# Optimization experiments

Hardware: AMD Instinct MI355X
Metric: run time of the kernel (lower is better)

Reference implementation:

```python
import jax, jax.numpy as jnp
import numpy as np
import math

IN_STACKS, IN_DIM, OUT_DIM = 4, 256, 2048
N_TOK = 16384


def _beta(a, b):
    return math.exp(math.lgamma(a) + math.lgamma(b) - math.lgamma(a + b))

BETA_NI = _beta(IN_DIM / 2.0, 0.5)
BETA_N = _beta(IN_DIM * IN_STACKS / 2.0, 0.5)


def sabs(x, eps=1e-15):
    return jnp.maximum(jnp.abs(x), eps)


def _project(x, k, eps=0.004):  # fp32 eps per source
    maxnorm = (1.0 - eps) / jnp.sqrt(sabs(k))
    maxnorm = jnp.where(k < 0, maxnorm, jnp.asarray(1e15, x.dtype))
    norm = jnp.maximum(jnp.linalg.norm(x, axis=-1, keepdims=True), 1e-15)
    return jnp.where(norm > maxnorm, x / norm * maxnorm, x)


def arsinh(x):
    return jnp.log(jnp.maximum(x + jnp.sqrt(1.0 + x * x), 1e-15))


def expmap0(u, c):
    sqrt_c = jnp.sqrt(c)
    un = jnp.maximum(jnp.linalg.norm(u, axis=-1, keepdims=True), 1e-15)
    gamma = jnp.tanh(sqrt_c * un) * u / (sqrt_c * un)
    return _project(gamma, -c)


def logmap0(y, c):
    sqrt_c = jnp.sqrt(c)
    yn = jnp.maximum(jnp.linalg.norm(y, axis=-1, keepdims=True), 1e-15)
    arg = jnp.minimum(sqrt_c * yn, 1.0 - 1e-7)
    return y / (sqrt_c * yn) * jnp.arctanh(arg)


def unidirectional_poincare_mlr(x, z_norm, z_unit, r, c):
    rc = jnp.sqrt(c)
    drcr = 2.0 * rc * r  # [out_dim]
    rcx = rc * x  # [N, D]
    cx2 = jnp.sum(rcx * rcx, axis=-1, keepdims=True)  # [N, 1]
    num = 2.0 * jnp.matmul(rcx, z_unit) * jnp.cosh(drcr) - (1.0 + cx2) * jnp.sinh(drcr)
    return 2.0 * z_norm / rc * arsinh(num / jnp.maximum(1.0 - cx2, 1e-15))


def poincare_linear(x, weight_g, z_unit, bias, c):
    rc = jnp.sqrt(c)
    y = unidirectional_poincare_mlr(x, weight_g, z_unit, bias, c)
    y = jnp.sinh(rc * y) / rc
    denom = 1.0 + jnp.sqrt(1.0 + c * jnp.sum(y * y, axis=-1, keepdims=True))
    return _project(y / denom, -c)


def setup_inputs() -> dict:
    key = jax.random.key(0)
    k1, k2 = jax.random.split(key)
    x = jax.random.normal(k1, (N_TOK, IN_STACKS, IN_DIM), dtype=jnp.float32)
    std = 1.0 / (2.0 * IN_DIM * IN_STACKS * OUT_DIM) ** 0.5
    weight_v = jax.random.normal(k2, (IN_STACKS * IN_DIM, OUT_DIM), dtype=jnp.float32) * std
    weight_g = jnp.linalg.norm(weight_v, axis=0)  # [OUT_DIM]
    bias = jnp.zeros((OUT_DIM,), dtype=jnp.float32)
    c = jnp.asarray(1.0, dtype=jnp.float32)
    return {"x": x, "weight_g": weight_g, "weight_v": weight_v, "bias": bias, "c": c}


def reference(x, weight_g, weight_v, bias, c):
    # x: [N, in_stacks, in_dim]
    xb = expmap0(x, c)
    xb = logmap0(xb, c).reshape(x.shape[0], IN_STACKS * IN_DIM)
    xb = expmap0(xb * (BETA_N / BETA_NI), c)
    z_unit = weight_v / jnp.maximum(jnp.linalg.norm(weight_v, axis=0), 1e-15)
    return poincare_linear(xb, weight_g, z_unit, bias, c)
```

## Files before the change

kernel.cpp:

```cpp
#include <hip/hip_runtime.h>
#include <hip/hip_bf16.h>
#include <hip/hip_fp16.h>
#include <cmath>

#define NTOK 16384
#define KDIM 1024
#define NDIM 2048
#define NSTK 4
#define SDIM 256

typedef __attribute__((ext_vector_type(8))) _Float16 f16x8;
typedef __attribute__((ext_vector_type(4))) float f32x4;

static __device__ __forceinline__ unsigned short f2h(float f) {
  union { _Float16 h; unsigned short u; } v;
  v.h = (_Float16)f;
  return v.u;
}

#define ASCL 16.0f
#define BSCL 32.0f
#define ABSCL 512.0f

__global__ void prep_cols(const float* __restrict__ wg, const float* __restrict__ bias,
                          const float* __restrict__ cptr, float* __restrict__ colp) {
  int j = blockIdx.x * 256 + threadIdx.x;
  if (j >= NDIM) return;
  float c = cptr[0];
  float rc = sqrtf(c);
  float w = wg[j];
  float invn = 1.0f / fmaxf(w, 1e-15f);
  float drcr = 2.0f * rc * bias[j];
  float ed = expf(drcr);
  float edi = 1.0f / ed;
  float coshd = 0.5f * (ed + edi);
  float sinhd = 0.5f * (ed - edi);
  colp[4 * j + 0] = 2.0f * invn * coshd / ABSCL;
  colp[4 * j + 1] = sinhd;
  colp[4 * j + 2] = 2.0f * w;
  colp[4 * j + 3] = 0.0f;
}

__global__ void transpose_w(const float* __restrict__ wv, unsigned short* __restrict__ Bt) {
  __shared__ float tile[32][33];
  int n0 = blockIdx.x * 32;
  int k0 = blockIdx.y * 32;
  int tx = threadIdx.x;
  int ty = threadIdx.y;
  for (int i = 0; i < 32; i += 8)
    tile[ty + i][tx] = wv[(long)(k0 + ty + i) * NDIM + n0 + tx];
  __syncthreads();
  for (int i = 0; i < 32; i += 8)
    Bt[(long)(n0 + ty + i) * KDIM + k0 + tx] = f2h(tile[tx][ty + i] * BSCL);
}

__global__ __launch_bounds__(256) void prep_x(const float* __restrict__ x, const float* __restrict__ cptr,
                                              unsigned short* __restrict__ A, float* __restrict__ cx2out,
                                              float Rbeta) {
  int w = threadIdx.x >> 6, lane = threadIdx.x & 63;
  int tok = blockIdx.x * 4 + w;
  const float4* x4 = (const float4*)x;
  float4 v[NSTK];
  float ss[NSTK];
  for (int s = 0; s < NSTK; s++) {
    float4 t = x4[(long)tok * 256 + s * 64 + lane];
    v[s] = t;
    float d = t.x * t.x + t.y * t.y + t.z * t.z + t.w * t.w;
    for (int m = 1; m < 64; m <<= 1) d += __shfl_xor(d, m);
    ss[s] = d;
  }
  float c = cptr[0];
  float rc = sqrtf(c);
  float h[NSTK], un[NSTK], hs2 = 0.0f;
  for (int s = 0; s < NSTK; s++) {
    un[s] = fmaxf(sqrtf(ss[s]), 1e-15f);
    float t1 = fminf(tanhf(rc * un[s]), 0.996f);
    float z = fminf(t1, 1.0f - 1e-7f);
    float hh = 0.5f * logf((1.0f + z) / (1.0f - z));
    h[s] = hh;
    hs2 += hh * hh;
  }
  float sqh = sqrtf(hs2);
  float uwrc = Rbeta * sqh;
  float t2 = fminf(tanhf(uwrc), 0.996f);
  if (lane == 0) cx2out[tok] = t2 * t2;
  float denomw = fmaxf(uwrc, rc * 1e-15f);
  for (int s = 0; s < NSTK; s++) {
    float scl = ASCL * Rbeta * h[s] * t2 / (un[s] * denomw);
    float4 t = v[s];
    ushort4 pk = make_ushort4(f2h(t.x * scl), f2h(t.y * scl), f2h(t.z * scl), f2h(t.w * scl));
    *(ushort4*)&A[(long)tok * KDIM + s * SDIM + lane * 4] = pk;
  }
}

#define BK 64
#define NKT (KDIM / BK)

#define GLDS16(g, l)                                                              \
  __builtin_amdgcn_global_load_lds((const __attribute__((address_space(1))) void*)(g), \
                                   (__attribute__((address_space(3))) void*)(l), 16, 0, 0)

#define PH_BARRIER __builtin_amdgcn_s_barrier()
#define PRIO1 __builtin_amdgcn_s_setprio(1)
#define PRIO0 __builtin_amdgcn_s_setprio(0)
#define LGKM0                                                  \
  do {                                                         \
    asm volatile("s_waitcnt lgkmcnt(0)" ::: "memory");         \
    __builtin_amdgcn_sched_barrier(0);                         \
  } while (0)
#define VMCNT4 asm volatile("s_waitcnt vmcnt(4)" ::: "memory")
#define VMCNT0 asm volatile("s_waitcnt vmcnt(0)" ::: "memory")

#define ISSUE_A(T, H)                                                        \
  do {                                                                       \
    const unsigned short* _s = Asrc + (long)(H) * (128 * KDIM) + (T) * BK;   \
    unsigned char* _d = lds + (((T) & 1) * 32768 + (H) * 16384) + tid * 16;  \
    GLDS16(_s, _d);                                                          \
    GLDS16(_s + 64 * KDIM, _d + 8192);                                       \
  } while (0)
#define ISSUE_B(T, H)                                                        \
  do {                                                                       \
    const unsigned short* _s = Bsrc + (long)(H) * (128 * KDIM) + (T) * BK;   \
    unsigned char* _d = lds + 65536 + (((T) & 1) * 32768 + (H) * 16384) + tid * 16; \
    GLDS16(_s, _d);                                                          \
    GLDS16(_s + 64 * KDIM, _d + 8192);                                       \
  } while (0)

#define READ_A4(BUFOFF, FMB, KS)                                             \
  _Pragma("unroll") for (int fm = 0; fm < 4; ++fm)                           \
    aF[fm][KS] = *(const f16x8*)(lds + (BUFOFF) + aBase + ((FMB) + fm) * 2048 + chunk[KS]);
#define READ_B4(BUFOFF, KS)                                                  \
  _Pragma("unroll") for (int fn = 0; fn < 4; ++fn)                           \
    bF[fn][KS] = *(const f16x8*)(lds + 65536 + (BUFOFF) + bBase + fn * 2048 + chunk[KS]);

#define MFMA_PH(FM0, KS)                                                     \
  _Pragma("unroll") for (int fi = 0; fi < 4; ++fi)                           \
    _Pragma("unroll") for (int fj = 0; fj < 4; ++fj)                         \
      acc[(FM0) + fi][fj] = __builtin_amdgcn_mfma_f32_16x16x32_f16(          \
          aF[fi][KS], bF[fj][KS], acc[(FM0) + fi][fj], 0, 0, 0);

#define TILE(BUFOFF, T, GA, GB, VMODE)                                       \
  do {                                                                       \
    READ_A4(BUFOFF, 0, 0); READ_B4(BUFOFF, 0);                               \
    if (GA) ISSUE_A((T) + 1, 0);                                             \
    PH_BARRIER; LGKM0;                                                       \
    PRIO1; MFMA_PH(0, 0); PRIO0;                                             \
    PH_BARRIER;                                                              \
    READ_A4(BUFOFF, 0, 1); READ_B4(BUFOFF, 1);                               \
    if (GA) ISSUE_A((T) + 1, 1);                                             \
    PH_BARRIER; LGKM0;                                                       \
    PRIO1; MFMA_PH(0, 1); PRIO0;                                             \
    PH_BARRIER;                                                              \
    READ_A4(BUFOFF, 4, 0);                                                   \
    if (GB) ISSUE_B((T) + 2, 0);                                             \
    PH_BARRIER; LGKM0;                                                       \
    PRIO1; MFMA_PH(4, 0); PRIO0;                                             \
    PH_BARRIER;                                                              \
    READ_A4(BUFOFF, 4, 1);                                                   \
    if (GB) ISSUE_B((T) + 2, 1);                                             \
    if ((VMODE) == 0) { VMCNT4; } else if ((VMODE) == 1) { VMCNT0; }         \
    PH_BARRIER; LGKM0;                                                       \
    PRIO1; MFMA_PH(4, 1); PRIO0;                                             \
    PH_BARRIER;                                                              \
  } while (0)

template <int F16S>
__global__ __launch_bounds__(512, 2) void gemm_ep(const unsigned short* __restrict__ A,
                                                  const unsigned short* __restrict__ Bt,
                                                  const float* __restrict__ cx2,
                                                  const float* __restrict__ colp,
                                                  const float* __restrict__ cptr,
                                                  float* __restrict__ outY,
                                                  unsigned short* __restrict__ y16,
                                                  float* __restrict__ partials) {
  __shared__ __attribute__((aligned(16))) unsigned char lds[131072];
  int tid = threadIdx.x;
  int lane = tid & 63, w = tid >> 6;
  int wm = w >> 2, wn = w & 3;
  int g = lane >> 4, r = lane & 15;
  int bid = blockIdx.x;
  int tile_n = bid & 7, tile_m = bid >> 3;
  int m0 = tile_m * 256, n0 = tile_n * 256;

  int srow = tid >> 3;
  int csrc = ((tid & 7) ^ (srow & 7)) << 3;
  const unsigned short* Asrc = A + (long)(m0 + srow) * KDIM + csrc;
  const unsigned short* Bsrc = Bt + (long)(n0 + srow) * KDIM + csrc;

  int aBase = wm * 16384 + r * 128;
  int bBase = (wn >> 1) * 16384 + (wn & 1) * 8192 + r * 128;
  int chunk[2];
  chunk[0] = ((0 * 4 + g) ^ (r & 7)) * 16;
  chunk[1] = ((1 * 4 + g) ^ (r & 7)) * 16;

  f32x4 acc[8][4];
#pragma unroll
  for (int i = 0; i < 8; i++)
#pragma unroll
    for (int j = 0; j < 4; j++) acc[i][j] = (f32x4){0.f, 0.f, 0.f, 0.f};
  f16x8 aF[4][2], bF[4][2];

  ISSUE_A(0, 0); ISSUE_A(0, 1); ISSUE_B(0, 0); ISSUE_B(0, 1);
  ISSUE_B(1, 0); ISSUE_B(1, 1);
  VMCNT4;
  PH_BARRIER;

#pragma unroll 1
  for (int it = 0; it < 7; ++it) {
    TILE(0, 2 * it, 1, 1, 0);
    TILE(32768, 2 * it + 1, 1, 1, 0);
  }
  TILE(0, 14, 1, 0, 1);
  TILE(32768, 15, 0, 0, 2);

  float c = cptr[0];
  float rc = sqrtf(c);
  float inv_rc = 1.0f / rc;
  const float4* cp4 = (const float4*)colp;
  int tn4 = tile_n * 4 + wn;
#pragma unroll
  for (int fm = 0; fm < 8; ++fm) {
#pragma unroll
    for (int q = 0; q < 4; ++q) {
      int row = m0 + wm * 128 + fm * 16 + g * 4 + q;
      float cx = cx2[row];
      float onec = 1.0f + cx;
      float rdn = 1.0f / fmaxf(1.0f - cx, 1e-15f);
      float rs = 0.0f;
#pragma unroll
      for (int fn = 0; fn < 4; ++fn) {
        int col = n0 + wn * 64 + fn * 16 + r;
        float4 cp = cp4[col];
        float dot = acc[fm][fn][q];
        float num = fmaf(dot, cp.x, -onec * cp.y);
        float u = num * rdn;
        float au = fabsf(u);
        float as = __logf(au + sqrtf(fmaf(au, au, 1.0f)));
        as = copysignf(as, u);
        float s2 = cp.z * as;
        float ex = __expf(s2);
        float exi = __builtin_amdgcn_rcpf(ex);
        float y = 0.5f * (ex - exi) * inv_rc;
        if (F16S)
          y16[(long)row * NDIM + col] = f2h(y);
        else
          outY[(long)row * NDIM + col] = y;
        rs = fmaf(y, y, rs);
      }
      rs += __shfl_xor(rs, 1);
      rs += __shfl_xor(rs, 2);
      rs += __shfl_xor(rs, 4);
      rs += __shfl_xor(rs, 8);
      if (r == 0) partials[(long)row * 32 + tn4] = rs;
    }
  }
}

__global__ __launch_bounds__(256) void finalize16(const unsigned short* __restrict__ y16,
                                                  const float* __restrict__ partials,
                                                  const float* __restrict__ cptr,
                                                  float* __restrict__ out) {
  int w = threadIdx.x >> 6, lane = threadIdx.x & 63;
  int row = blockIdx.x * 4 + w;
  float p = (lane < 32) ? partials[(long)row * 32 + lane] : 0.0f;
  for (int m = 1; m < 64; m <<= 1) p += __shfl_xor(p, m);
  float c = cptr[0];
  float S = p;
  float denom = 1.0f + sqrtf(fmaf(c, S, 1.0f));
  float nv = fmaxf(sqrtf(S) / denom, 1e-15f);
  float maxn = (c > 0.0f) ? 0.996f / sqrtf(fmaxf(c, 1e-15f)) : 1e15f;
  float scl = (nv > maxn) ? (maxn / (nv * denom)) : (1.0f / denom);
  const f16x8* yr = (const f16x8*)(y16 + (long)row * NDIM);
  float4* o4 = (float4*)(out + (long)row * NDIM);
#pragma unroll
  for (int it = 0; it < 4; ++it) {
    f16x8 v = yr[it * 64 + lane];
    float4 a, b;
    a.x = (float)v[0] * scl; a.y = (float)v[1] * scl;
    a.z = (float)v[2] * scl; a.w = (float)v[3] * scl;
    b.x = (float)v[4] * scl; b.y = (float)v[5] * scl;
    b.z = (float)v[6] * scl; b.w = (float)v[7] * scl;
    o4[(it * 64 + lane) * 2] = a;
    o4[(it * 64 + lane) * 2 + 1] = b;
  }
}

__global__ __launch_bounds__(256) void finalize32(float* __restrict__ out,
                                                  const float* __restrict__ partials,
                                                  const float* __restrict__ cptr) {
  int w = threadIdx.x >> 6, lane = threadIdx.x & 63;
  int row = blockIdx.x * 4 + w;
  float p = (lane < 32) ? partials[(long)row * 32 + lane] : 0.0f;
  for (int m = 1; m < 64; m <<= 1) p += __shfl_xor(p, m);
  float c = cptr[0];
  float S = p;
  float denom = 1.0f + sqrtf(fmaf(c, S, 1.0f));
  float nv = fmaxf(sqrtf(S) / denom, 1e-15f);
  float maxn = (c > 0.0f) ? 0.996f / sqrtf(fmaxf(c, 1e-15f)) : 1e15f;
  float scl = (nv > maxn) ? (maxn / (nv * denom)) : (1.0f / denom);
  float4* o4 = (float4*)(out + (long)row * NDIM);
  for (int it = 0; it < NDIM / 256; ++it) {
    float4 v = o4[it * 64 + lane];
    v.x *= scl; v.y *= scl; v.z *= scl; v.w *= scl;
    o4[it * 64 + lane] = v;
  }
}

extern "C" void kernel_launch(void* const* d_in, const int* in_sizes, int n_in,
                              void* d_out, int out_size, void* d_ws, size_t ws_size,
                              hipStream_t stream) {
  const float* x = (const float*)d_in[0];
  const float* wg = (const float*)d_in[1];
  const float* wv = (const float*)d_in[2];
  const float* bias = (const float*)d_in[3];
  const float* cpt = (const float*)d_in[4];
  float* out = (float*)d_out;

  char* ws = (char*)d_ws;
  unsigned short* A = (unsigned short*)ws;
  unsigned short* Bt = (unsigned short*)(ws + 33554432);
  float* cx2 = (float*)(ws + 37748736);
  float* colp = (float*)(ws + 37814272);
  float* parts = (float*)(ws + 37847040);
  unsigned short* Y16 = (unsigned short*)(ws + 39944192);
  const size_t NEED_F16S = 39944192ull + 67108864ull;

  double lbni = lgamma(128.0) + lgamma(0.5) - lgamma(128.5);
  double lbn = lgamma(512.0) + lgamma(0.5) - lgamma(512.5);
  float Rbeta = (float)exp(lbn - lbni);

  prep_cols<<<8, 256, 0, stream>>>(wg, bias, cpt, colp);
  transpose_w<<<dim3(64, 32), dim3(32, 8), 0, stream>>>(wv, Bt);
  prep_x<<<4096, 256, 0, stream>>>(x, cpt, A, cx2, Rbeta);
  if (ws_size >= NEED_F16S) {
    gemm_ep<1><<<512, 512, 0, stream>>>(A, Bt, cx2, colp, cpt, out, Y16, parts);
    finalize16<<<4096, 256, 0, stream>>>(Y16, parts, cpt, out);
  } else {
    gemm_ep<0><<<512, 512, 0, stream>>>(A, Bt, cx2, colp, cpt, out, Y16, parts);
    finalize32<<<4096, 256, 0, stream>>>(out, parts, cpt);
  }
}
```

Before: 183.6 us.

## Stage fp16 epilogue through swizzled LDS for 16-byte coalesced global stores

The GEMM epilogue now writes each wave's fp16 y values into a per-wave XOR-swizzled LDS region, then reads them back as 8-element vectors and stores full 128-byte row segments to global memory instead of scattered 2-byte stores. It also replaces __logf/__expf with the native log2/exp2 builtins, which cancel the ln/ln2 scaling, and applies the sign once at the end. This targets the store-transaction overhead of the epilogue. It relies on the LDS tile buffers being free after the main loop (only a per-wave lgkmcnt wait, no block barrier) and on 16KB of LDS per wave.

```diff
diff --git a/kernel.cpp b/kernel.cpp
--- a/kernel.cpp
+++ b/kernel.cpp
@@ -218,33 +218,36 @@
   float inv_rc = 1.0f / rc;
   const float4* cp4 = (const float4*)colp;
   int tn4 = tile_n * 4 + wn;
+  unsigned char* wlds = &lds[w * 16384];
 #pragma unroll
   for (int fm = 0; fm < 8; ++fm) {
 #pragma unroll
     for (int q = 0; q < 4; ++q) {
-      int row = m0 + wm * 128 + fm * 16 + g * 4 + q;
+      int rw = fm * 16 + g * 4 + q;
+      int row = m0 + wm * 128 + rw;
       float cx = cx2[row];
       float onec = 1.0f + cx;
       float rdn = 1.0f / fmaxf(1.0f - cx, 1e-15f);
       float rs = 0.0f;
+      int rmask = ((rw >> 1) & 7) << 3;
 #pragma unroll
       for (int fn = 0; fn < 4; ++fn) {
-        int col = n0 + wn * 64 + fn * 16 + r;
+        int cw = fn * 16 + r;
+        int col = n0 + wn * 64 + cw;
         float4 cp = cp4[col];
         float dot = acc[fm][fn][q];
         float num = fmaf(dot, cp.x, -onec * cp.y);
         float u = num * rdn;
         float au = fabsf(u);
-        float as = __logf(au + sqrtf(fmaf(au, au, 1.0f)));
-        as = copysignf(as, u);
-        float s2 = cp.z * as;
-        float ex = __expf(s2);
+        float l2 = __builtin_amdgcn_logf(au + sqrtf(fmaf(au, au, 1.0f)));
+        float ex = __builtin_amdgcn_exp2f(cp.z * l2);
         float exi = __builtin_amdgcn_rcpf(ex);
-        float y = 0.5f * (ex - exi) * inv_rc;
-        if (F16S)
-          y16[(long)row * NDIM + col] = f2h(y);
-        else
+        float y = copysignf(0.5f * (ex - exi) * inv_rc, u);
+        if (F16S) {
+          *(unsigned short*)(wlds + rw * 128 + ((cw ^ rmask) << 1)) = f2h(y);
+        } else {
           outY[(long)row * NDIM + col] = y;
+        }
         rs = fmaf(y, y, rs);
       }
       rs += __shfl_xor(rs, 1);
@@ -252,6 +255,19 @@
       rs += __shfl_xor(rs, 4);
       rs += __shfl_xor(rs, 8);
       if (r == 0) partials[(long)row * 32 + tn4] = rs;
+    }
+  }
+  if (F16S) {
+    asm volatile("s_waitcnt lgkmcnt(0)" ::: "memory");
+    __builtin_amdgcn_sched_barrier(0);
+    int rsub = lane >> 3;
+    int cw0 = (lane & 7) * 8;
+#pragma unroll
+    for (int it2 = 0; it2 < 16; ++it2) {
+      int rw = it2 * 8 + rsub;
+      int rmask = ((rw >> 1) & 7) << 3;
+      f16x8 v = *(const f16x8*)(wlds + rw * 128 + ((cw0 ^ rmask) << 1));
+      *(f16x8*)&y16[(long)(m0 + wm * 128 + rw) * NDIM + n0 + wn * 64 + cw0] = v;
     }
   }
 }
```

After: 173.4 us. -5.6%, faster.
